# Kernel optimization log

Hardware: AMD Instinct MI355X
Metric: run time of the kernel (lower is better)

The kernel has to match this reference:

```python
import jax, jax.numpy as jnp
import numpy as np

STRIDES = (4, 8, 16, 32)   # featmap_strides (FPN levels)
TAU = 2.0                  # level-weight temperature (translate_to_linear_weight)
G = 4                      # n_groups
SP = 32                    # spatial_points
TP = 8                     # temporal_points == T frames
D = 256                    # query_dim == feat_channels
CG = D // G                # channels per group
EFF = CG                   # eff_in_dim == eff_out_dim in AdaptiveMixing
OUT_S = SP * 4             # out_points (spatial), out_multiplier = 4
OUT_T = TP * 4
B, Q, T, IMG = 4, 100, 8, 256


def _ln2(x, eps=1e-5):
    # F.layer_norm over the last TWO dims, no affine params
    mu = jnp.mean(x, axis=(-2, -1), keepdims=True)
    var = jnp.var(x, axis=(-2, -1), keepdims=True)
    return (x - mu) * jax.lax.rsqrt(var + eps)


def _ln(x, g, b, eps=1e-5):
    mu = jnp.mean(x, axis=-1, keepdims=True)
    var = jnp.var(x, axis=-1, keepdims=True)
    return (x - mu) * jax.lax.rsqrt(var + eps) * g + b


def _bilinear(feat, px, py):
    # feat: [B,H,W,T,G,Cg]; px,py: [B,Q,G,S] pixel coords
    # grid_sample semantics: bilinear, align_corners=False, zero padding
    Bn, H, W, Tn, Gn, Cg = feat.shape
    bidx = jnp.arange(Bn)[:, None, None, None]
    gidx = jnp.arange(Gn)[None, None, :, None]
    x0 = jnp.floor(px); y0 = jnp.floor(py)
    fx = px - x0; fy = py - y0
    x0i = x0.astype(jnp.int32); y0i = y0.astype(jnp.int32)
    out = 0.0
    for dx, dy, w in ((0, 0, (1 - fx) * (1 - fy)), (1, 0, fx * (1 - fy)),
                      (0, 1, (1 - fx) * fy), (1, 1, fx * fy)):
        xi = x0i + dx; yi = y0i + dy
        valid = (xi >= 0) & (xi < W) & (yi >= 0) & (yi < H)
        xc = jnp.clip(xi, 0, W - 1); yc = jnp.clip(yi, 0, H - 1)
        v = feat[bidx, yc, xc, :, gidx, :]   # [B,Q,G,S,T,Cg]
        out = out + v * (w * valid)[..., None, None]
    return out


def _adaptive_mixing(x, query, Wp, bp, Wo, bo, n_in, n_out):
    # x: [B,Q,G,P,Cg]; per-instance dynamic channel mixing then point mixing
    Bn, Qn = x.shape[:2]
    params = (query @ Wp + bp).reshape(Bn, Qn, G, -1)
    M = params[..., :EFF * EFF].reshape(Bn, Qn, G, EFF, EFF)
    S = params[..., EFF * EFF:].reshape(Bn, Qn, G, n_out, n_in)
    out = jnp.einsum('bqgpc,bqgcd->bqgpd', x, M)
    out = jax.nn.relu(_ln2(out))
    out = jnp.einsum('bqgop,bqgpd->bqgod', S, out)
    out = jax.nn.relu(_ln2(out))
    out = out.reshape(Bn, Qn, -1) @ Wo + bo
    return query + out


def _forward(feat0, feat1, feat2, feat3, proposal_boxes, spatial_queries, temporal_queries,
             W_off, b_off, W_ps, b_ps, Wo_s, bo_s, g_s, be_s,
             W_pt, b_pt, Wo_t, bo_t, g_t, be_t):
    feats = (feat0, feat1, feat2, feat3)
    Bn, Qn, _ = spatial_queries.shape
    # offset_generator + make_sample_points (xyzr proposal boxes)
    off = (spatial_queries @ W_off + b_off).reshape(Bn, Qn, G * SP, 3)
    cc = proposal_boxes[..., None, :2]
    scale = 2.0 ** proposal_boxes[..., None, 2:3]
    r = proposal_boxes[..., None, 3:4]
    wh = scale * jnp.concatenate([2.0 ** (-0.5 * r), 2.0 ** (0.5 * r)], axis=-1)
    xy = (cc + off[..., :2] * wh).reshape(Bn, Qn, G, SP, 2)
    z = (proposal_boxes[..., None, 2] + off[..., 2]).reshape(Bn, Qn, G, SP)
    # soft level weights over log2-scale distance (translate_to_linear_weight)
    mapped = z - jnp.float32(float(np.log2(STRIDES[0])))
    lvls = jnp.arange(len(STRIDES), dtype=z.dtype)
    lw = jax.nn.softmax(-((mapped[..., None] - lvls) ** 2) / TAU, axis=-1)
    sampled = 0.0
    for i, feat in enumerate(feats):
        Bc, C, Tn, H, W = feat.shape
        fr = feat.transpose(0, 3, 4, 2, 1).reshape(Bc, H, W, Tn, G, CG)
        px = xy[..., 0] / STRIDES[i] - 0.5
        py = xy[..., 1] / STRIDES[i] - 0.5
        sampled = sampled + _bilinear(fr, px, py) * lw[..., i][..., None, None]
    sampled = sampled.transpose(0, 1, 2, 4, 3, 5)     # [B,Q,G,T,SP,Cg]
    spatial_feats = jnp.mean(sampled, axis=3)         # mean over T   -> [B,Q,G,SP,Cg]
    temporal_feats = jnp.mean(sampled, axis=4)        # mean over SP  -> [B,Q,G,T,Cg]
    sq = _adaptive_mixing(spatial_feats, spatial_queries, W_ps, b_ps, Wo_s, bo_s, SP, OUT_S)
    sq = _ln(sq, g_s, be_s)
    tq = _adaptive_mixing(temporal_feats, temporal_queries, W_pt, b_pt, Wo_t, bo_t, TP, OUT_T)
    tq = _ln(tq, g_t, be_t)
    return sq, tq


def setup_inputs() -> dict:
    key = jax.random.key(0)
    ks = jax.random.split(key, 24)
    f32 = jnp.float32
    inp = {}
    for i, s in enumerate(STRIDES):
        h = IMG // s
        inp['feat%d' % i] = jax.random.normal(ks[i], (B, D, T, h, h), dtype=f32)
    # xyzr boxes: center xy in image coords, z = log2 box scale, r = log2 aspect
    inp['proposal_boxes'] = jnp.concatenate([
        jax.random.uniform(ks[4], (B, Q, 2), dtype=f32) * IMG,
        jax.random.uniform(ks[5], (B, Q, 1), dtype=f32) * 3.0 + 3.0,
        jax.random.normal(ks[6], (B, Q, 1), dtype=f32) * 0.25,
    ], axis=-1)
    PS = EFF * EFF + SP * OUT_S
    PT = EFF * EFF + TP * OUT_T
    inp.update(
        spatial_queries=jax.random.normal(ks[7], (B, Q, D), dtype=f32),
        temporal_queries=jax.random.normal(ks[8], (B, Q, D), dtype=f32),
        W_off=jax.random.normal(ks[9], (D, SP * G * 3), dtype=f32) * 0.01,
        b_off=jax.random.normal(ks[10], (SP * G * 3,), dtype=f32) * 0.1,
        W_ps=jax.random.normal(ks[11], (D, G * PS), dtype=f32) * 0.02,
        b_ps=jax.random.normal(ks[12], (G * PS,), dtype=f32) * 0.02,
        Wo_s=jax.random.normal(ks[13], (G * EFF * OUT_S, D), dtype=f32) * 0.02,
        bo_s=jax.random.normal(ks[14], (D,), dtype=f32) * 0.02,
        g_s=jnp.ones((D,), dtype=f32),
        be_s=jnp.zeros((D,), dtype=f32),
        W_pt=jax.random.normal(ks[15], (D, G * PT), dtype=f32) * 0.02,
        b_pt=jax.random.normal(ks[16], (G * PT,), dtype=f32) * 0.02,
        Wo_t=jax.random.normal(ks[17], (G * EFF * OUT_T, D), dtype=f32) * 0.02,
        bo_t=jax.random.normal(ks[18], (D,), dtype=f32) * 0.02,
        g_t=jnp.ones((D,), dtype=f32),
        be_t=jnp.zeros((D,), dtype=f32),
    )
    return inp


def reference(feat0, feat1, feat2, feat3, proposal_boxes, spatial_queries, temporal_queries,
              W_off, b_off, W_ps, b_ps, Wo_s, bo_s, g_s, be_s,
              W_pt, b_pt, Wo_t, bo_t, g_t, be_t):
    return _forward(feat0, feat1, feat2, feat3, proposal_boxes, spatial_queries, temporal_queries,
                    W_off, b_off, W_ps, b_ps, Wo_s, bo_s, g_s, be_s,
                    W_pt, b_pt, Wo_t, bo_t, g_t, be_t)
```

## Files before the change

kernel.cpp:

```cpp
#include <hip/hip_runtime.h>
#include <hip/hip_bf16.h>


typedef __attribute__((ext_vector_type(8))) short bf16x8;
typedef __attribute__((ext_vector_type(8))) unsigned short u16x8;
typedef __attribute__((ext_vector_type(4))) float f32x4;

static __device__ __forceinline__ unsigned short f2bf(float f){
  unsigned u = __float_as_uint(f);
  u += 0x7fffu + ((u >> 16) & 1u);
  return (unsigned short)(u >> 16);
}
static __device__ __forceinline__ float bf2f(unsigned short h){
  return __uint_as_float(((unsigned)h) << 16);
}

__global__ __launch_bounds__(256) void k_wtrans_all(
    const float* __restrict__ Wps, const float* __restrict__ Wpt,
    const float* __restrict__ Wos, const float* __restrict__ Wot,
    unsigned short* __restrict__ WpsP, unsigned short* __restrict__ WptP,
    unsigned short* __restrict__ WosP, unsigned short* __restrict__ WotP,
    const float4* __restrict__ qs, const float4* __restrict__ qt,
    unsigned short* __restrict__ qsP, unsigned short* __restrict__ qtP){
  int id = blockIdx.x;
  if(id >= 5696){
    int blk = id - 5696;
    const float4* in; unsigned short* out; int i;
    if(blk < 100){ in = qs; out = qsP; i = blk*256 + threadIdx.x; }
    else         { in = qt; out = qtP; i = (blk-100)*256 + threadIdx.x; }
    float4 v = in[i];
    int row = i >> 6, k0 = (i & 63) * 4;
    int strip = row >> 4, colr = row & 15;
    int kk = k0 >> 5, kg = (k0 >> 3) & 3, e0 = k0 & 7;
    size_t dst = ((size_t)(strip*8 + kk)*64 + kg*16 + colr)*8 + e0;
    *(ushort4*)(out + dst) = make_ushort4(f2bf(v.x), f2bf(v.y), f2bf(v.z), f2bf(v.w));
    return;
  }
  const float* in; unsigned short* out; int N, KKtot, r0, c0;
  if(id < 2048){       in=Wps; out=WpsP; N=32768; KKtot=8;    c0=(id>>2)*64;        r0=(id&3)*64; }
  else if(id < 3136){ int i=id-2048; in=Wpt; out=WptP; N=17408; KKtot=8;    c0=(i>>2)*64; r0=(i&3)*64; }
  else if(id < 5184){ int i=id-3136; in=Wos; out=WosP; N=256;   KKtot=1024; c0=(i&3)*64;  r0=(i>>2)*64; }
  else {              int i=id-5184; in=Wot; out=WotP; N=256;   KKtot=256;  c0=(i&3)*64;  r0=(i>>2)*64; }
  __shared__ float tile[64][65];
  int lane = threadIdx.x & 63, wid = threadIdx.x >> 6;
  #pragma unroll
  for(int i=0;i<16;i++){
    int r = wid + 4*i;
    tile[r][lane] = in[(size_t)(r0 + r) * N + c0 + lane];
  }
  __syncthreads();
  int t = threadIdx.x;
  int ch = t >> 5, w2 = t & 31;
  int kk_l = ch >> 2, st_l = ch & 3;
  size_t chunkbase = ((size_t)((c0>>4) + st_l) * KKtot + ((r0>>5) + kk_l)) * 512;
  #pragma unroll
  for(int j=0;j<2;j++){
    int pl = w2*2 + j;
    int kg = pl >> 4, cc = pl & 15;
    u16x8 v;
    #pragma unroll
    for(int e=0;e<8;e++) v[e] = f2bf(tile[kk_l*32 + kg*8 + e][st_l*16 + cc]);
    *(u16x8*)(out + chunkbase + pl*8) = v;
  }
}

__global__ __launch_bounds__(256) void k_feat_transpose_all(
    const float* __restrict__ f0, const float* __restrict__ f1,
    const float* __restrict__ f2, const float* __restrict__ f3,
    unsigned short* __restrict__ o0, unsigned short* __restrict__ o1,
    unsigned short* __restrict__ o2, unsigned short* __restrict__ o3){
  int px = blockIdx.x;
  const float* in; unsigned short* out; int P, p0;
  if(px < 64){      in=f0; out=o0; P=4096; p0=px*64; }
  else if(px < 80){ in=f1; out=o1; P=1024; p0=(px-64)*64; }
  else if(px < 84){ in=f2; out=o2; P=256;  p0=(px-80)*64; }
  else {            in=f3; out=o3; P=64;   p0=0; }
  __shared__ float tile[64][65];
  int c0 = blockIdx.y * 64;
  int b = blockIdx.z >> 3, t = blockIdx.z & 7;
  int tid = threadIdx.x;
  size_t inbase = ((size_t)b * 2048 + t) * (size_t)P;
  #pragma unroll
  for(int j=0;j<4;j++){
    int idx = j*256 + tid;
    int c = idx >> 4, q4 = idx & 15;
    float4 v = *(const float4*)(in + inbase + (size_t)(c0 + c) * 8 * P + p0 + q4*4);
    tile[c][q4*4+0] = v.x; tile[c][q4*4+1] = v.y;
    tile[c][q4*4+2] = v.z; tile[c][q4*4+3] = v.w;
  }
  __syncthreads();
  size_t outbase = (size_t)b * P * 2048 + (size_t)t * 256;
  #pragma unroll
  for(int j=0;j<4;j++){
    int idx = j*256 + tid;
    int p = idx >> 4, q4 = idx & 15;
    ushort4 o;
    o.x = f2bf(tile[q4*4+0][p]); o.y = f2bf(tile[q4*4+1][p]);
    o.z = f2bf(tile[q4*4+2][p]); o.w = f2bf(tile[q4*4+3][p]);
    *(ushort4*)(out + outbase + (size_t)(p0 + p) * 2048 + c0 + q4*4) = o;
  }
}

__global__ __launch_bounds__(384) void k_offsets(
    const float* __restrict__ q, const float* __restrict__ Woff,
    const float* __restrict__ boff, const float* __restrict__ boxes,
    int2* __restrict__ tapbuf){
  int bq = blockIdx.x;
  __shared__ float qsh[256];
  __shared__ float off[384];
  int tid = threadIdx.x;
  if(tid < 256) qsh[tid] = q[bq*256 + tid];
  __syncthreads();
  float acc = boff[tid];
  for(int k=0;k<256;k++) acc = fmaf(qsh[k], Woff[k*384 + tid], acc);
  off[tid] = acc;
  __syncthreads();
  if(tid < 128){
    float cx = boxes[bq*4+0], cy = boxes[bq*4+1];
    float zb = boxes[bq*4+2], r  = boxes[bq*4+3];
    float wx = exp2f(zb - 0.5f*r);
    float wy = exp2f(zb + 0.5f*r);
    float x = cx + off[tid*3+0]*wx;
    float y = cy + off[tid*3+1]*wy;
    float z = zb + off[tid*3+2];
    float m = z - 2.0f;
    float e0 = -0.5f*(m-0.f)*(m-0.f);
    float e1 = -0.5f*(m-1.f)*(m-1.f);
    float e2 = -0.5f*(m-2.f)*(m-2.f);
    float e3 = -0.5f*(m-3.f)*(m-3.f);
    float mx = fmaxf(fmaxf(e0,e1), fmaxf(e2,e3));
    float s0 = expf(e0-mx), s1 = expf(e1-mx), s2 = expf(e2-mx), s3 = expf(e3-mx);
    float inv = 1.0f/(s0+s1+s2+s3);
    float lwv[4] = {s0*inv, s1*inv, s2*inv, s3*inv};
    const int abase[4] = {0, 67108864, 83886080, 88080384};
    const int bsize[4] = {16777216, 4194304, 1048576, 262144};
    int b = bq / 100;
    int2* tp = tapbuf + ((size_t)bq*128 + tid)*16;
    #pragma unroll
    for(int l=0;l<4;l++){
      float invs = (l==0) ? 0.25f : (l==1) ? 0.125f : (l==2) ? 0.0625f : 0.03125f;
      int W = 64 >> l;
      float px = x*invs - 0.5f, py = y*invs - 0.5f;
      float x0f = floorf(px), y0f = floorf(py);
      int x0 = (int)x0f, y0 = (int)y0f;
      float fx = px - x0f, fy = py - y0f;
      int lb = abase[l] + b*bsize[l];
      #pragma unroll
      for(int tap=0; tap<4; tap++){
        int dx = tap & 1, dy = tap >> 1;
        int xi = x0 + dx, yi = y0 + dy;
        bool valid = (xi >= 0) & (xi < W) & (yi >= 0) & (yi < W);
        int xc = min(max(xi, 0), W-1), yc = min(max(yi, 0), W-1);
        float w = (dx ? fx : 1.f-fx) * (dy ? fy : 1.f-fy) * lwv[l];
        tp[l*4 + tap] = make_int2(lb + (yc*W + xc)*4096,
                                  __float_as_int(valid ? w : 0.f));
      }
    }
  }
}

__global__ __launch_bounds__(256, 4) void k_sample_params(
    const unsigned short* __restrict__ arena,
    const int2* __restrict__ tapbuf,
    float* __restrict__ sfeat, float* __restrict__ tfeat,
    const unsigned short* __restrict__ As, const unsigned short* __restrict__ WTs,
    const float* __restrict__ biass, unsigned short* __restrict__ outs,
    const unsigned short* __restrict__ At, const unsigned short* __restrict__ WTt,
    const float* __restrict__ biast, unsigned short* __restrict__ outt){
  if(blockIdx.x >= 1600){
    int flat = blockIdx.x - 1600;
    int nb = flat % 784, my = flat / 784;
    const unsigned short *A, *W; const float* bias; unsigned short* out; int N, nbl;
    if(nb < 512){ A=As; W=WTs; bias=biass; out=outs; N=32768; nbl=nb; }
    else        { A=At; W=WTt; bias=biast; out=outt; N=17408; nbl=nb-512; }
    int wave = threadIdx.x >> 6, lane = threadIdx.x & 63;
    int strip = nbl*4 + wave;
    int col = lane & 15, kg = lane >> 4;
    const bf16x8* wp = (const bf16x8*)W + (size_t)strip*8*64 + lane;
    bf16x8 bfrag[8];
    #pragma unroll
    for(int k=0;k<8;k++) bfrag[k] = wp[k*64];
    float bv = bias[strip*16 + col];
    int mt0 = my * 5;
    #pragma unroll
    for(int m=0; m<5; m++){
      int mt = mt0 + m;
      f32x4 acc = {bv, bv, bv, bv};
      const bf16x8* ap = (const bf16x8*)A + (size_t)mt*8*64 + lane;
      bf16x8 af[8];
      #pragma unroll
      for(int k=0;k<8;k++) af[k] = ap[k*64];
      #pragma unroll
      for(int k=0;k<8;k++)
        acc = __builtin_amdgcn_mfma_f32_16x16x32_bf16(af[k], bfrag[k], acc, 0, 0, 0);
      int rowb = mt*16 + kg*4;
      #pragma unroll
      for(int r=0;r<4;r++)
        out[(size_t)(rowb + r) * N + strip*16 + col] = f2bf(acc[r]);
    }
    return;
  }
  int bid = blockIdx.x;
  int g = bid & 3, bq = bid >> 2;
  __shared__ unsigned smp[32][8][32];
  int tid = threadIdx.x;
  int cp = tid & 31, t = tid >> 5;
  int tcb = t*512 + g*128 + cp*4;
  const char* ar = (const char*)arena;
  const int2* tb = tapbuf + (size_t)(bq*128 + g*32)*16;
  float t0 = 0.f, t1 = 0.f;
  #pragma unroll 2
  for(int sp=0; sp<32; sp++){
    float a0 = 0.f, a1 = 0.f;
    #pragma unroll
    for(int j=0; j<16; j++){
      int2 td = tb[sp*16 + j];
      float w = __int_as_float(td.y);
      unsigned v = *(const unsigned*)(ar + (size_t)(unsigned)td.x + tcb);
      a0 = fmaf(w, __uint_as_float((v & 0xffffu) << 16), a0);
      a1 = fmaf(w, __uint_as_float(v & 0xffff0000u),      a1);
    }
    smp[sp][t][cp] = (unsigned)f2bf(a0) | ((unsigned)f2bf(a1) << 16);
    t0 += a0; t1 += a1;
  }
  __syncthreads();
  {
    size_t o = ((size_t)(bq*4 + g)*8 + t)*64 + cp*2;
    tfeat[o+0] = t0 * (1.f/32.f);
    tfeat[o+1] = t1 * (1.f/32.f);
  }
  #pragma unroll
  for(int i=0;i<4;i++){
    int j = tid + 256*i;
    int sp = j >> 5, p = j & 31;
    float s0 = 0.f, s1 = 0.f;
    #pragma unroll
    for(int tt=0; tt<8; tt++){
      unsigned v = smp[sp][tt][p];
      s0 += __uint_as_float((v & 0xffffu) << 16);
      s1 += __uint_as_float(v & 0xffff0000u);
    }
    size_t o = ((size_t)(bq*4 + g)*32 + sp)*64 + p*2;
    sfeat[o+0] = s0 * 0.125f;
    sfeat[o+1] = s1 * 0.125f;
  }
}

static __device__ __forceinline__ void block_reduce2(
    float& s1, float& s2, float* rA, float* rB, int tid){
  #pragma unroll
  for(int o=32;o;o>>=1){ s1 += __shfl_xor(s1,o); s2 += __shfl_xor(s2,o); }
  int wave = tid >> 6, lane = tid & 63;
  if(lane == 0){ rA[wave] = s1; rB[wave] = s2; }
  __syncthreads();
  s1 = rA[0]+rA[1]+rA[2]+rA[3];
  s2 = rB[0]+rB[1]+rB[2]+rB[3];
}

template<int P, int O>
static __device__ void mix_body(
    float* shbuf, const float* __restrict__ feats,
    const unsigned short* __restrict__ params,
    unsigned short* __restrict__ hidden, int KK, int bid){
  int g = bid & 3, bq = bid >> 2;
  const int PG = 4096 + O*P;
  const unsigned short* pp = params + (size_t)bq * 4 * PG + (size_t)g * PG;
  const float* xin = feats + (size_t)(bq*4 + g) * P * 64;
  float (*xs)[64] = (float(*)[64])shbuf;
  float (*o1)[64] = (float(*)[64])(shbuf + P*64);
  float* Ss = shbuf + 2*P*64;
  float* rA = shbuf + 2*P*64 + O*P;
  float* rB = rA + 4;
  int tid = threadIdx.x; int d = tid & 63; int pb = tid >> 6;
  for(int i=tid; i<P*64; i+=256) xs[i>>6][i&63] = xin[i];
  for(int i=tid; i<O*P; i+=256) Ss[i] = bf2f(pp[4096 + i]);
  __syncthreads();
  constexpr int NP = P/4;
  float a[NP];
  #pragma unroll
  for(int i=0;i<NP;i++) a[i] = 0.f;
  for(int c=0;c<64;c++){
    float mv = bf2f(pp[c*64 + d]);
    #pragma unroll
    for(int i=0;i<NP;i++) a[i] = fmaf(xs[pb + 4*i][c], mv, a[i]);
  }
  float s1 = 0.f, s2 = 0.f;
  #pragma unroll
  for(int i=0;i<NP;i++){ s1 += a[i]; s2 += a[i]*a[i]; }
  block_reduce2(s1, s2, rA, rB, tid);
  {
    const float n = (float)(P*64);
    float mu = s1/n, var = s2/n - mu*mu;
    float rstd = rsqrtf(var + 1e-5f);
    #pragma unroll
    for(int i=0;i<NP;i++){
      float v = (a[i] - mu) * rstd;
      o1[pb + 4*i][d] = fmaxf(v, 0.f);
    }
  }
  __syncthreads();
  constexpr int NO = O/4;
  float bacc[NO];
  #pragma unroll
  for(int i=0;i<NO;i++){
    float acc = 0.f;
    int o = pb + 4*i;
    #pragma unroll
    for(int p=0;p<P;p++) acc = fmaf(Ss[o*P + p], o1[p][d], acc);
    bacc[i] = acc;
  }
  s1 = 0.f; s2 = 0.f;
  #pragma unroll
  for(int i=0;i<NO;i++){ s1 += bacc[i]; s2 += bacc[i]*bacc[i]; }
  block_reduce2(s1, s2, rA, rB, tid);
  {
    const float n = (float)(O*64);
    float mu = s1/n, var = s2/n - mu*mu;
    float rstd = rsqrtf(var + 1e-5f);
    int strip = bq >> 4, colr = bq & 15;
    int kg = (d >> 3) & 3, e = d & 7, dh = d >> 5;
    #pragma unroll
    for(int i=0;i<NO;i++){
      int o = pb + 4*i;
      float v = (bacc[i] - mu) * rstd;
      int kk = (g*O + o)*2 + dh;
      size_t addr = ((size_t)(strip*KK + kk)*64 + kg*16 + colr)*8 + e;
      hidden[addr] = f2bf(fmaxf(v, 0.f));
    }
  }
}

__global__ __launch_bounds__(256) void k_mix_all(
    const float* __restrict__ sfeat, const unsigned short* __restrict__ params_s,
    unsigned short* __restrict__ hid_s,
    const float* __restrict__ tfeat, const unsigned short* __restrict__ params_t,
    unsigned short* __restrict__ hid_t){
  __shared__ float shbuf[2*32*64 + 128*32 + 8];
  if(blockIdx.x < 1600)
    mix_body<32,128>(shbuf, sfeat, params_s, hid_s, 1024, blockIdx.x);
  else
    mix_body<8,32>(shbuf, tfeat, params_t, hid_t, 256, blockIdx.x - 1600);
}

__global__ __launch_bounds__(256, 4) void k_gemm_final(
    const unsigned short* __restrict__ Hs, const unsigned short* __restrict__ WTs,
    float* __restrict__ parts, const unsigned short* __restrict__ Ht,
    const unsigned short* __restrict__ WTt, float* __restrict__ partt){
  const unsigned short *H, *W; float* partial; int KK, ks, ksteps;
  if(blockIdx.x < 32){ H=Hs; W=WTs; partial=parts; KK=1024; ks=blockIdx.x;    ksteps=32; }
  else               { H=Ht; W=WTt; partial=partt; KK=256;  ks=blockIdx.x-32; ksteps=8;  }
  int wave = threadIdx.x >> 6, lane = threadIdx.x & 63;
  int col = lane & 15, kg = lane >> 4;
  int mt = blockIdx.y;
  int kk0 = ks * ksteps;
  int n0 = wave * 64;
  f32x4 acc[4] = {};
  const bf16x8* ap  = (const bf16x8*)H + ((size_t)mt*KK + kk0)*64 + lane;
  const bf16x8* bp0 = (const bf16x8*)W + ((size_t)(4*wave+0)*KK + kk0)*64 + lane;
  const bf16x8* bp1 = (const bf16x8*)W + ((size_t)(4*wave+1)*KK + kk0)*64 + lane;
  const bf16x8* bp2 = (const bf16x8*)W + ((size_t)(4*wave+2)*KK + kk0)*64 + lane;
  const bf16x8* bp3 = (const bf16x8*)W + ((size_t)(4*wave+3)*KK + kk0)*64 + lane;
  #pragma unroll 4
  for(int kk=0; kk<ksteps; kk++){
    bf16x8 af = ap[kk*64];
    bf16x8 b0 = bp0[kk*64], b1 = bp1[kk*64], b2 = bp2[kk*64], b3 = bp3[kk*64];
    acc[0] = __builtin_amdgcn_mfma_f32_16x16x32_bf16(af, b0, acc[0], 0,0,0);
    acc[1] = __builtin_amdgcn_mfma_f32_16x16x32_bf16(af, b1, acc[1], 0,0,0);
    acc[2] = __builtin_amdgcn_mfma_f32_16x16x32_bf16(af, b2, acc[2], 0,0,0);
    acc[3] = __builtin_amdgcn_mfma_f32_16x16x32_bf16(af, b3, acc[3], 0,0,0);
  }
  int rowb = mt*16 + kg*4;
  #pragma unroll
  for(int nt=0; nt<4; nt++)
    #pragma unroll
    for(int r=0; r<4; r++)
      partial[((size_t)ks*400 + rowb + r)*256 + n0 + nt*16 + col] = acc[nt][r];
}

template<int NS>
__global__ __launch_bounds__(256) void k_finalize(
    const float* __restrict__ part_s, const float* __restrict__ part_t,
    const float* __restrict__ qs, const float* __restrict__ qt,
    const float* __restrict__ bos, const float* __restrict__ bot,
    const float* __restrict__ gs, const float* __restrict__ gt,
    const float* __restrict__ bes, const float* __restrict__ bet,
    float* __restrict__ out_s, float* __restrict__ out_t){
  __shared__ float rA[4], rB[4];
  int bq = blockIdx.x, j = threadIdx.x;
  const float *partial, *q, *bo, *gam, *bet_;
  float* out;
  if(blockIdx.y == 0){ partial=part_s; q=qs; bo=bos; gam=gs; bet_=bes; out=out_s; }
  else               { partial=part_t; q=qt; bo=bot; gam=gt; bet_=bet; out=out_t; }
  float v = q[bq*256 + j] + bo[j];
  #pragma unroll 8
  for(int s=0;s<NS;s++) v += partial[((size_t)s*400 + bq)*256 + j];
  float s1 = v, s2 = v*v;
  block_reduce2(s1, s2, rA, rB, j);
  float mu = s1 * (1.f/256.f);
  float var = s2 * (1.f/256.f) - mu*mu;
  float rstd = rsqrtf(var + 1e-5f);
  out[bq*256 + j] = (v - mu) * rstd * gam[j] + bet_[j];
}

extern "C" void kernel_launch(void* const* d_in, const int* in_sizes, int n_in,
                              void* d_out, int out_size, void* d_ws, size_t ws_size,
                              hipStream_t stream){
  const float* feat0 = (const float*)d_in[0];
  const float* feat1 = (const float*)d_in[1];
  const float* feat2 = (const float*)d_in[2];
  const float* feat3 = (const float*)d_in[3];
  const float* boxes = (const float*)d_in[4];
  const float* qs    = (const float*)d_in[5];
  const float* qt    = (const float*)d_in[6];
  const float* Woff  = (const float*)d_in[7];
  const float* boff  = (const float*)d_in[8];
  const float* Wps   = (const float*)d_in[9];
  const float* bps   = (const float*)d_in[10];
  const float* Wos   = (const float*)d_in[11];
  const float* bos   = (const float*)d_in[12];
  const float* gs    = (const float*)d_in[13];
  const float* bes   = (const float*)d_in[14];
  const float* Wpt   = (const float*)d_in[15];
  const float* bpt   = (const float*)d_in[16];
  const float* Wot   = (const float*)d_in[17];
  const float* bot   = (const float*)d_in[18];
  const float* gt    = (const float*)d_in[19];
  const float* bet   = (const float*)d_in[20];

  char* ws = (char*)d_ws;
  unsigned short* featT0 = (unsigned short*)(ws + 0);
  unsigned short* featT1 = (unsigned short*)(ws + 67108864);
  unsigned short* featT2 = (unsigned short*)(ws + 83886080);
  unsigned short* featT3 = (unsigned short*)(ws + 88080384);
  float* part_s          = (float*)(ws + 0);
  float* part_t          = (float*)(ws + 52428800);
  unsigned short* qsP    = (unsigned short*)(ws + 89128960);
  unsigned short* qtP    = (unsigned short*)(ws + 89333760);
  unsigned short* WpsP   = (unsigned short*)(ws + 89538560);
  unsigned short* WptP   = (unsigned short*)(ws + 106315776);
  unsigned short* WosP   = (unsigned short*)(ws + 115228672);
  unsigned short* WotP   = (unsigned short*)(ws + 132005888);
  float* sfeat           = (float*)(ws + 137461760);
  float* tfeat           = (float*)(ws + 150568960);
  unsigned short* hid_s  = (unsigned short*)(ws + 153845760);
  unsigned short* hid_t  = (unsigned short*)(ws + 180060160);
  unsigned short* params_s = (unsigned short*)(ws + 186613760);
  unsigned short* params_t = (unsigned short*)(ws + 212828160);
  int2* tapbuf           = (int2*)(ws + 226754560);
  float* out_s = (float*)d_out;
  float* out_t = out_s + 102400;

  k_wtrans_all<<<5896, 256, 0, stream>>>(Wps, Wpt, Wos, Wot, WpsP, WptP, WosP, WotP,
                                         (const float4*)qs, (const float4*)qt, qsP, qtP);
  k_feat_transpose_all<<<dim3(85, 4, 32), 256, 0, stream>>>(
      feat0, feat1, feat2, feat3, featT0, featT1, featT2, featT3);
  k_offsets<<<400, 384, 0, stream>>>(qs, Woff, boff, boxes, tapbuf);
  k_sample_params<<<5520, 256, 0, stream>>>(featT0, tapbuf, sfeat, tfeat,
                                            qsP, WpsP, bps, params_s,
                                            qtP, WptP, bpt, params_t);
  k_mix_all<<<3200, 256, 0, stream>>>(sfeat, params_s, hid_s,
                                      tfeat, params_t, hid_t);
  k_gemm_final<<<dim3(64, 25), 256, 0, stream>>>(hid_s, WosP, part_s,
                                                 hid_t, WotP, part_t);
  k_finalize<32><<<dim3(400, 2), 256, 0, stream>>>(
      part_s, part_t, qs, qt, bos, bot, gs, gt, bes, bet, out_s, out_t);
}
```

Baseline: 285.9 us.

## Group-major feature arena layout and merge prep kernels into one launch

Merges the weight/query transposes and the feature transposes into one k_prep launch. It also changes the bf16 feature arena from pixel-major with all groups interleaved to group-major, with a per-group block per level. Tap offsets and the sampler's channel offset are recomputed so each group's 8-frame by 64-channel vector for a pixel is contiguous (1 KB instead of spread across 4 KB). This aims to improve cache locality of the gather in the sampling kernel and to remove one launch. The merged kernel now carries launch_bounds(256,4) and more branch dispatch.

New measurement: 267.1 us. -6.6%, faster.

```diff
diff --git a/kernel.cpp b/kernel.cpp
--- a/kernel.cpp
+++ b/kernel.cpp
@@ -15,89 +15,96 @@
   return __uint_as_float(((unsigned)h) << 16);
 }
 
-__global__ __launch_bounds__(256) void k_wtrans_all(
+__global__ __launch_bounds__(256, 4) void k_prep(
+    const float* __restrict__ f0, const float* __restrict__ f1,
+    const float* __restrict__ f2, const float* __restrict__ f3,
+    unsigned short* __restrict__ arena,
     const float* __restrict__ Wps, const float* __restrict__ Wpt,
     const float* __restrict__ Wos, const float* __restrict__ Wot,
     unsigned short* __restrict__ WpsP, unsigned short* __restrict__ WptP,
     unsigned short* __restrict__ WosP, unsigned short* __restrict__ WotP,
-    const float4* __restrict__ qs, const float4* __restrict__ qt,
+    const float4* __restrict__ qs4, const float4* __restrict__ qt4,
     unsigned short* __restrict__ qsP, unsigned short* __restrict__ qtP){
+  __shared__ float tile[64][65];
   int id = blockIdx.x;
-  if(id >= 5696){
-    int blk = id - 5696;
+  int tid = threadIdx.x;
+
+  if(id < 10880){
+    int px = id % 85, rest = id / 85;
+    int g = rest & 3;
+    int z = rest >> 2;
+    int b = z >> 3, t = z & 7;
+    const float* in; int P, p0, l;
+    if(px < 64){      in=f0; P=4096; p0=px*64;      l=0; }
+    else if(px < 80){ in=f1; P=1024; p0=(px-64)*64; l=1; }
+    else if(px < 84){ in=f2; P=256;  p0=(px-80)*64; l=2; }
+    else {            in=f3; P=64;   p0=0;          l=3; }
+    const size_t base_us[4]  = {0, 33554432, 41943040, 44040192};
+    const size_t gsize_us[4] = {8388608, 2097152, 524288, 131072};
+    int c0 = g*64;
+    size_t inbase = ((size_t)b * 2048 + t) * (size_t)P;
+    #pragma unroll
+    for(int j=0;j<4;j++){
+      int idx = j*256 + tid;
+      int c = idx >> 4, q4 = idx & 15;
+      float4 v = *(const float4*)(in + inbase + (size_t)(c0 + c) * 8 * P + p0 + q4*4);
+      tile[c][q4*4+0] = v.x; tile[c][q4*4+1] = v.y;
+      tile[c][q4*4+2] = v.z; tile[c][q4*4+3] = v.w;
+    }
+    __syncthreads();
+    unsigned short* out = arena + base_us[l] + g*gsize_us[l];
+    #pragma unroll
+    for(int j=0;j<4;j++){
+      int idx = j*256 + tid;
+      int p = idx >> 4, q4 = idx & 15;
+      ushort4 o;
+      o.x = f2bf(tile[q4*4+0][p]); o.y = f2bf(tile[q4*4+1][p]);
+      o.z = f2bf(tile[q4*4+2][p]); o.w = f2bf(tile[q4*4+3][p]);
+      *(ushort4*)(out + ((size_t)(b*P + p0 + p)*8 + t)*64 + q4*4) = o;
+    }
+    return;
+  }
+
+  if(id < 16576){
+    int wi = id - 10880;
+    const float* in; unsigned short* out; int N, KKtot, r0, c0;
+    if(wi < 2048){       in=Wps; out=WpsP; N=32768; KKtot=8;    c0=(wi>>2)*64;        r0=(wi&3)*64; }
+    else if(wi < 3136){ int i2=wi-2048; in=Wpt; out=WptP; N=17408; KKtot=8;    c0=(i2>>2)*64; r0=(i2&3)*64; }
+    else if(wi < 5184){ int i2=wi-3136; in=Wos; out=WosP; N=256;   KKtot=1024; c0=(i2&3)*64;  r0=(i2>>2)*64; }
+    else {              int i2=wi-5184; in=Wot; out=WotP; N=256;   KKtot=256;  c0=(i2&3)*64;  r0=(i2>>2)*64; }
+    int lane = tid & 63, wid = tid >> 6;
+    #pragma unroll
+    for(int i2=0;i2<16;i2++){
+      int r = wid + 4*i2;
+      tile[r][lane] = in[(size_t)(r0 + r) * N + c0 + lane];
+    }
+    __syncthreads();
+    int ch = tid >> 5, w2 = tid & 31;
+    int kk_l = ch >> 2, st_l = ch & 3;
+    size_t chunkbase = ((size_t)((c0>>4) + st_l) * KKtot + ((r0>>5) + kk_l)) * 512;
+    #pragma unroll
+    for(int j=0;j<2;j++){
+      int pl = w2*2 + j;
+      int kg = pl >> 4, cc = pl & 15;
+      u16x8 v;
+      #pragma unroll
+      for(int e=0;e<8;e++) v[e] = f2bf(tile[kk_l*32 + kg*8 + e][st_l*16 + cc]);
+      *(u16x8*)(out + chunkbase + pl*8) = v;
+    }
+    return;
+  }
+
+  {
+    int blk = id - 16576;
     const float4* in; unsigned short* out; int i;
-    if(blk < 100){ in = qs; out = qsP; i = blk*256 + threadIdx.x; }
-    else         { in = qt; out = qtP; i = (blk-100)*256 + threadIdx.x; }
+    if(blk < 100){ in = qs4; out = qsP; i = blk*256 + tid; }
+    else         { in = qt4; out = qtP; i = (blk-100)*256 + tid; }
     float4 v = in[i];
     int row = i >> 6, k0 = (i & 63) * 4;
     int strip = row >> 4, colr = row & 15;
     int kk = k0 >> 5, kg = (k0 >> 3) & 3, e0 = k0 & 7;
     size_t dst = ((size_t)(strip*8 + kk)*64 + kg*16 + colr)*8 + e0;
     *(ushort4*)(out + dst) = make_ushort4(f2bf(v.x), f2bf(v.y), f2bf(v.z), f2bf(v.w));
-    return;
-  }
-  const float* in; unsigned short* out; int N, KKtot, r0, c0;
-  if(id < 2048){       in=Wps; out=WpsP; N=32768; KKtot=8;    c0=(id>>2)*64;        r0=(id&3)*64; }
-  else if(id < 3136){ int i=id-2048; in=Wpt; out=WptP; N=17408; KKtot=8;    c0=(i>>2)*64; r0=(i&3)*64; }
-  else if(id < 5184){ int i=id-3136; in=Wos; out=WosP; N=256;   KKtot=1024; c0=(i&3)*64;  r0=(i>>2)*64; }
-  else {              int i=id-5184; in=Wot; out=WotP; N=256;   KKtot=256;  c0=(i&3)*64;  r0=(i>>2)*64; }
-  __shared__ float tile[64][65];
-  int lane = threadIdx.x & 63, wid = threadIdx.x >> 6;
-  #pragma unroll
-  for(int i=0;i<16;i++){
-    int r = wid + 4*i;
-    tile[r][lane] = in[(size_t)(r0 + r) * N + c0 + lane];
-  }
-  __syncthreads();
-  int t = threadIdx.x;
-  int ch = t >> 5, w2 = t & 31;
-  int kk_l = ch >> 2, st_l = ch & 3;
-  size_t chunkbase = ((size_t)((c0>>4) + st_l) * KKtot + ((r0>>5) + kk_l)) * 512;
-  #pragma unroll
-  for(int j=0;j<2;j++){
-    int pl = w2*2 + j;
-    int kg = pl >> 4, cc = pl & 15;
-    u16x8 v;
-    #pragma unroll
-    for(int e=0;e<8;e++) v[e] = f2bf(tile[kk_l*32 + kg*8 + e][st_l*16 + cc]);
-    *(u16x8*)(out + chunkbase + pl*8) = v;
-  }
-}
-
-__global__ __launch_bounds__(256) void k_feat_transpose_all(
-    const float* __restrict__ f0, const float* __restrict__ f1,
-    const float* __restrict__ f2, const float* __restrict__ f3,
-    unsigned short* __restrict__ o0, unsigned short* __restrict__ o1,
-    unsigned short* __restrict__ o2, unsigned short* __restrict__ o3){
-  int px = blockIdx.x;
-  const float* in; unsigned short* out; int P, p0;
-  if(px < 64){      in=f0; out=o0; P=4096; p0=px*64; }
-  else if(px < 80){ in=f1; out=o1; P=1024; p0=(px-64)*64; }
-  else if(px < 84){ in=f2; out=o2; P=256;  p0=(px-80)*64; }
-  else {            in=f3; out=o3; P=64;   p0=0; }
-  __shared__ float tile[64][65];
-  int c0 = blockIdx.y * 64;
-  int b = blockIdx.z >> 3, t = blockIdx.z & 7;
-  int tid = threadIdx.x;
-  size_t inbase = ((size_t)b * 2048 + t) * (size_t)P;
-  #pragma unroll
-  for(int j=0;j<4;j++){
-    int idx = j*256 + tid;
-    int c = idx >> 4, q4 = idx & 15;
-    float4 v = *(const float4*)(in + inbase + (size_t)(c0 + c) * 8 * P + p0 + q4*4);
-    tile[c][q4*4+0] = v.x; tile[c][q4*4+1] = v.y;
-    tile[c][q4*4+2] = v.z; tile[c][q4*4+3] = v.w;
-  }
-  __syncthreads();
-  size_t outbase = (size_t)b * P * 2048 + (size_t)t * 256;
-  #pragma unroll
-  for(int j=0;j<4;j++){
-    int idx = j*256 + tid;
-    int p = idx >> 4, q4 = idx & 15;
-    ushort4 o;
-    o.x = f2bf(tile[q4*4+0][p]); o.y = f2bf(tile[q4*4+1][p]);
-    o.z = f2bf(tile[q4*4+2][p]); o.w = f2bf(tile[q4*4+3][p]);
-    *(ushort4*)(out + outbase + (size_t)(p0 + p) * 2048 + c0 + q4*4) = o;
   }
 }
 
@@ -133,8 +140,10 @@
     float inv = 1.0f/(s0+s1+s2+s3);
     float lwv[4] = {s0*inv, s1*inv, s2*inv, s3*inv};
     const int abase[4] = {0, 67108864, 83886080, 88080384};
-    const int bsize[4] = {16777216, 4194304, 1048576, 262144};
+    const int gsize[4] = {16777216, 4194304, 1048576, 262144};
+    const int bsize[4] = {4194304, 1048576, 262144, 65536};
     int b = bq / 100;
+    int g = tid >> 5;
     int2* tp = tapbuf + ((size_t)bq*128 + tid)*16;
     #pragma unroll
     for(int l=0;l<4;l++){
@@ -144,7 +153,7 @@
       float x0f = floorf(px), y0f = floorf(py);
       int x0 = (int)x0f, y0 = (int)y0f;
       float fx = px - x0f, fy = py - y0f;
-      int lb = abase[l] + b*bsize[l];
+      int lb = abase[l] + g*gsize[l] + b*bsize[l];
       #pragma unroll
       for(int tap=0; tap<4; tap++){
         int dx = tap & 1, dy = tap >> 1;
@@ -152,7 +161,7 @@
         bool valid = (xi >= 0) & (xi < W) & (yi >= 0) & (yi < W);
         int xc = min(max(xi, 0), W-1), yc = min(max(yi, 0), W-1);
         float w = (dx ? fx : 1.f-fx) * (dy ? fy : 1.f-fy) * lwv[l];
-        tp[l*4 + tap] = make_int2(lb + (yc*W + xc)*4096,
+        tp[l*4 + tap] = make_int2(lb + (yc*W + xc)*1024,
                                   __float_as_int(valid ? w : 0.f));
       }
     }
@@ -205,7 +214,7 @@
   __shared__ unsigned smp[32][8][32];
   int tid = threadIdx.x;
   int cp = tid & 31, t = tid >> 5;
-  int tcb = t*512 + g*128 + cp*4;
+  int tcb = t*128 + cp*4;
   const char* ar = (const char*)arena;
   const int2* tb = tapbuf + (size_t)(bq*128 + g*32)*16;
   float t0 = 0.f, t1 = 0.f;
@@ -428,10 +437,7 @@
   const float* bet   = (const float*)d_in[20];
 
   char* ws = (char*)d_ws;
-  unsigned short* featT0 = (unsigned short*)(ws + 0);
-  unsigned short* featT1 = (unsigned short*)(ws + 67108864);
-  unsigned short* featT2 = (unsigned short*)(ws + 83886080);
-  unsigned short* featT3 = (unsigned short*)(ws + 88080384);
+  unsigned short* arena  = (unsigned short*)(ws + 0);
   float* part_s          = (float*)(ws + 0);
   float* part_t          = (float*)(ws + 52428800);
   unsigned short* qsP    = (unsigned short*)(ws + 89128960);
@@ -450,12 +456,11 @@
   float* out_s = (float*)d_out;
   float* out_t = out_s + 102400;
 
-  k_wtrans_all<<<5896, 256, 0, stream>>>(Wps, Wpt, Wos, Wot, WpsP, WptP, WosP, WotP,
-                                         (const float4*)qs, (const float4*)qt, qsP, qtP);
-  k_feat_transpose_all<<<dim3(85, 4, 32), 256, 0, stream>>>(
-      feat0, feat1, feat2, feat3, featT0, featT1, featT2, featT3);
+  k_prep<<<16776, 256, 0, stream>>>(feat0, feat1, feat2, feat3, arena,
+                                    Wps, Wpt, Wos, Wot, WpsP, WptP, WosP, WotP,
+                                    (const float4*)qs, (const float4*)qt, qsP, qtP);
   k_offsets<<<400, 384, 0, stream>>>(qs, Woff, boff, boxes, tapbuf);
-  k_sample_params<<<5520, 256, 0, stream>>>(featT0, tapbuf, sfeat, tfeat,
+  k_sample_params<<<5520, 256, 0, stream>>>(arena, tapbuf, sfeat, tfeat,
                                             qsP, WpsP, bps, params_s,
                                             qtP, WptP, bpt, params_t);
   k_mix_all<<<3200, 256, 0, stream>>>(sfeat, params_s, hid_s,
```

## Reorder transposed feature arena to group-major layout for sampling locality

Applied to the files above, without the earlier changes.

The feature transpose now writes each FPN level as [group][batch][pixel][time][64 channels] instead of [batch][pixel][time*256 channels]. The offset kernel folds the group into the tap base address and uses a 1024-byte pixel stride, and the sampler drops the group term from its per-thread offset. Each group's sampling block then reads a contiguous 1KB chunk per tap, which should improve cache-line use and locality for the gather. The transpose's writes become narrower (64 channels per pixel/time row), which may change store efficiency.

After: 282.2 us. About the same (-1.3%).

```diff
diff --git a/kernel.cpp b/kernel.cpp
--- a/kernel.cpp
+++ b/kernel.cpp
@@ -64,20 +64,23 @@
   }
 }
 
-__global__ __launch_bounds__(256) void k_feat_transpose_all(
+__global__ __launch_bounds__(256) void k_ftrans(
     const float* __restrict__ f0, const float* __restrict__ f1,
     const float* __restrict__ f2, const float* __restrict__ f3,
-    unsigned short* __restrict__ o0, unsigned short* __restrict__ o1,
-    unsigned short* __restrict__ o2, unsigned short* __restrict__ o3){
+    unsigned short* __restrict__ arena){
   int px = blockIdx.x;
-  const float* in; unsigned short* out; int P, p0;
-  if(px < 64){      in=f0; out=o0; P=4096; p0=px*64; }
-  else if(px < 80){ in=f1; out=o1; P=1024; p0=(px-64)*64; }
-  else if(px < 84){ in=f2; out=o2; P=256;  p0=(px-80)*64; }
-  else {            in=f3; out=o3; P=64;   p0=0; }
+  int g = blockIdx.y;
+  int z = blockIdx.z;
+  int b = z >> 3, t = z & 7;
+  const float* in; int P, p0, l;
+  if(px < 64){      in=f0; P=4096; p0=px*64;      l=0; }
+  else if(px < 80){ in=f1; P=1024; p0=(px-64)*64; l=1; }
+  else if(px < 84){ in=f2; P=256;  p0=(px-80)*64; l=2; }
+  else {            in=f3; P=64;   p0=0;          l=3; }
+  const size_t base_us[4]  = {0, 33554432, 41943040, 44040192};
+  const size_t gsize_us[4] = {8388608, 2097152, 524288, 131072};
   __shared__ float tile[64][65];
-  int c0 = blockIdx.y * 64;
-  int b = blockIdx.z >> 3, t = blockIdx.z & 7;
+  int c0 = g*64;
   int tid = threadIdx.x;
   size_t inbase = ((size_t)b * 2048 + t) * (size_t)P;
   #pragma unroll
@@ -89,7 +92,7 @@
     tile[c][q4*4+2] = v.z; tile[c][q4*4+3] = v.w;
   }
   __syncthreads();
-  size_t outbase = (size_t)b * P * 2048 + (size_t)t * 256;
+  unsigned short* out = arena + base_us[l] + g*gsize_us[l];
   #pragma unroll
   for(int j=0;j<4;j++){
     int idx = j*256 + tid;
@@ -97,7 +100,7 @@
     ushort4 o;
     o.x = f2bf(tile[q4*4+0][p]); o.y = f2bf(tile[q4*4+1][p]);
     o.z = f2bf(tile[q4*4+2][p]); o.w = f2bf(tile[q4*4+3][p]);
-    *(ushort4*)(out + outbase + (size_t)(p0 + p) * 2048 + c0 + q4*4) = o;
+    *(ushort4*)(out + ((size_t)(b*P + p0 + p)*8 + t)*64 + q4*4) = o;
   }
 }
 
@@ -133,8 +136,10 @@
     float inv = 1.0f/(s0+s1+s2+s3);
     float lwv[4] = {s0*inv, s1*inv, s2*inv, s3*inv};
     const int abase[4] = {0, 67108864, 83886080, 88080384};
-    const int bsize[4] = {16777216, 4194304, 1048576, 262144};
+    const int gsize[4] = {16777216, 4194304, 1048576, 262144};
+    const int bsize[4] = {4194304, 1048576, 262144, 65536};
     int b = bq / 100;
+    int g = tid >> 5;
     int2* tp = tapbuf + ((size_t)bq*128 + tid)*16;
     #pragma unroll
     for(int l=0;l<4;l++){
@@ -144,7 +149,7 @@
       float x0f = floorf(px), y0f = floorf(py);
       int x0 = (int)x0f, y0 = (int)y0f;
       float fx = px - x0f, fy = py - y0f;
-      int lb = abase[l] + b*bsize[l];
+      int lb = abase[l] + g*gsize[l] + b*bsize[l];
       #pragma unroll
       for(int tap=0; tap<4; tap++){
         int dx = tap & 1, dy = tap >> 1;
@@ -152,7 +157,7 @@
         bool valid = (xi >= 0) & (xi < W) & (yi >= 0) & (yi < W);
         int xc = min(max(xi, 0), W-1), yc = min(max(yi, 0), W-1);
         float w = (dx ? fx : 1.f-fx) * (dy ? fy : 1.f-fy) * lwv[l];
-        tp[l*4 + tap] = make_int2(lb + (yc*W + xc)*4096,
+        tp[l*4 + tap] = make_int2(lb + (yc*W + xc)*1024,
                                   __float_as_int(valid ? w : 0.f));
       }
     }
@@ -205,7 +210,7 @@
   __shared__ unsigned smp[32][8][32];
   int tid = threadIdx.x;
   int cp = tid & 31, t = tid >> 5;
-  int tcb = t*512 + g*128 + cp*4;
+  int tcb = t*128 + cp*4;
   const char* ar = (const char*)arena;
   const int2* tb = tapbuf + (size_t)(bq*128 + g*32)*16;
   float t0 = 0.f, t1 = 0.f;
@@ -428,10 +433,7 @@
   const float* bet   = (const float*)d_in[20];
 
   char* ws = (char*)d_ws;
-  unsigned short* featT0 = (unsigned short*)(ws + 0);
-  unsigned short* featT1 = (unsigned short*)(ws + 67108864);
-  unsigned short* featT2 = (unsigned short*)(ws + 83886080);
-  unsigned short* featT3 = (unsigned short*)(ws + 88080384);
+  unsigned short* arena  = (unsigned short*)(ws + 0);
   float* part_s          = (float*)(ws + 0);
   float* part_t          = (float*)(ws + 52428800);
   unsigned short* qsP    = (unsigned short*)(ws + 89128960);
@@ -452,10 +454,9 @@
 
   k_wtrans_all<<<5896, 256, 0, stream>>>(Wps, Wpt, Wos, Wot, WpsP, WptP, WosP, WotP,
                                          (const float4*)qs, (const float4*)qt, qsP, qtP);
-  k_feat_transpose_all<<<dim3(85, 4, 32), 256, 0, stream>>>(
-      feat0, feat1, feat2, feat3, featT0, featT1, featT2, featT3);
+  k_ftrans<<<dim3(85, 4, 32), 256, 0, stream>>>(feat0, feat1, feat2, feat3, arena);
   k_offsets<<<400, 384, 0, stream>>>(qs, Woff, boff, boxes, tapbuf);
-  k_sample_params<<<5520, 256, 0, stream>>>(featT0, tapbuf, sfeat, tfeat,
+  k_sample_params<<<5520, 256, 0, stream>>>(arena, tapbuf, sfeat, tfeat,
                                             qsP, WpsP, bps, params_s,
                                             qtP, WptP, bpt, params_t);
   k_mix_all<<<3200, 256, 0, stream>>>(sfeat, params_s, hid_s,
```
